# Optimization experiments

Measured on AMD Instinct MI355X. Metric: run time of the kernel, lower is better.

## Reference

```python
import jax, jax.numpy as jnp
import numpy as np

# Band partition of the 2049 frequency bins (BSRNN-style: narrow low bands, wide high bands)
_WIDTHS = [25] * 10 + [50] * 12 + [100] * 8 + [399]
_STARTS = np.concatenate([[0], np.cumsum(_WIDTHS)])
SUBBANDS = [(int(_STARTS[i]), int(_STARTS[i + 1])) for i in range(len(_WIDTHS))]
C_IN = 2          # stereo complex input channels
OUT_CH = 128      # band embedding dim
EPS = 1e-5        # GroupNorm eps
TOTAL_CH = sum(2 * C_IN * (e - s) for s, e in SUBBANDS)  # 8196


def setup_inputs() -> dict:
    key = jax.random.key(0)
    k1, k2, k3, k4 = jax.random.split(key, 4)
    B, F, T = 8, 2049, 512
    # x is view_as_real of a complex spectrogram: [B, C, F, T, 2]
    x = jax.random.normal(k1, (B, C_IN, F, T), dtype=jnp.float32)
    x = jnp.stack([x, jax.random.normal(k2, (B, C_IN, F, T), dtype=jnp.float32)], axis=-1)
    gamma = jax.random.uniform(k3, (TOTAL_CH,), dtype=jnp.float32)            # GroupNorm weight (concat over bands)
    beta = jax.random.normal(k4, (TOTAL_CH,), dtype=jnp.float32) * 0.1       # GroupNorm bias
    W = jax.random.normal(jax.random.fold_in(key, 5), (OUT_CH, TOTAL_CH), dtype=jnp.float32) * 0.02  # 1x1 conv weights, concat over bands
    b = jax.random.normal(jax.random.fold_in(key, 6), (len(SUBBANDS), OUT_CH), dtype=jnp.float32) * 0.02
    return {"x": x, "gamma": gamma, "beta": beta, "W": W, "b": b}


def reference(x, gamma, beta, W, b):
    # x: [B, C, F, T, 2] (real view of complex spectrogram)
    B, C, F, T, _ = x.shape
    outs = []
    off = 0
    for i, (s, e) in enumerate(SUBBANDS):
        ch = 2 * C * (e - s)
        # moveaxis(-1, 1): [B, 2, C, w, T] -> reshape [B, 2*C*w, T]
        h = jnp.moveaxis(x[:, :, s:e, :, :], -1, 1).reshape(B, ch, T)
        # GroupNorm(1, ch): normalize over (channel, time) per sample
        mu = jnp.mean(h, axis=(1, 2), keepdims=True)
        var = jnp.var(h, axis=(1, 2), keepdims=True)
        g = gamma[off:off + ch][None, :, None]
        bt = beta[off:off + ch][None, :, None]
        hn = (h - mu) * jax.lax.rsqrt(var + EPS) * g + bt
        # 1x1 Conv1d == per-timestep linear: [out, ch] x [B, ch, T] -> [B, out, T]
        y = jnp.einsum('oc,bct->bot', W[:, off:off + ch], hn) + b[i][None, :, None]
        outs.append(y)
        off += ch
    return jnp.stack(outs, axis=2)  # [B, OUT_CH, n_bands, T]
```

## Files before the change

### kernel.cpp

```cpp
#include <hip/hip_runtime.h>
#include <hip/hip_bf16.h>

typedef __attribute__((ext_vector_type(8))) short short8;
typedef __attribute__((ext_vector_type(4))) float f32x4;

#define NBANDS 31
#define BB 8
#define CCH 2
#define FF 2049
#define TTS 512
#define OUTC 128
#define TCH 8196
#define EPSV 1e-5f

__constant__ int c_wid[NBANDS] = {
    25,25,25,25,25,25,25,25,25,25,
    50,50,50,50,50,50,50,50,50,50,50,50,
    100,100,100,100,100,100,100,100,
    399};
__constant__ int c_start[NBANDS] = {
    0,25,50,75,100,125,150,175,200,225,
    250,300,350,400,450,500,550,600,650,700,750,800,
    850,950,1050,1150,1250,1350,1450,1550,
    1650};
__constant__ int c_cumf[NBANDS + 1] = {
    0,1,2,3,4,5,6,7,8,9,
    10,12,14,16,18,20,22,24,26,28,30,32,
    34,38,42,46,50,54,58,62,
    66,79};
__constant__ int c_kpad[NBANDS] = {
    128,128,128,128,128,128,128,128,128,128,
    256,256,256,256,256,256,256,256,256,256,256,256,
    448,448,448,448,448,448,448,448,
    1600};
__constant__ int c_kbase[NBANDS] = {
    0,16384,32768,49152,65536,81920,98304,114688,131072,147456,
    163840,196608,229376,262144,294912,327680,360448,393216,425984,458752,491520,524288,
    557056,614400,671744,729088,786432,843776,901120,958464,
    1015808};
__constant__ int c_order[NBANDS] = {
    30,22,23,24,25,26,27,28,29,
    10,11,12,13,14,15,16,17,18,19,20,21,
    0,1,2,3,4,5,6,7,8,9};

#define NSTATS 1264
#define NWPREP 248
#define NWP2   992

__device__ inline unsigned short f2bf(float f) {
    __hip_bfloat16 h = __float2bfloat16(f);
    unsigned short u;
    __builtin_memcpy(&u, &h, 2);
    return u;
}

__device__ inline void gload_lds16(const void* g, void* l) {
    __builtin_amdgcn_global_load_lds((const __attribute__((address_space(1))) void*)g,
                                     (__attribute__((address_space(3))) void*)l, 16, 0, 0);
}

__global__ __launch_bounds__(256) void prep(const float* __restrict__ x,
                                            const float* __restrict__ W,
                                            const float* __restrict__ gamma,
                                            const float* __restrict__ beta,
                                            const float* __restrict__ bias,
                                            float* __restrict__ st,
                                            float* __restrict__ wgam,
                                            float* __restrict__ wcb,
                                            unsigned short* __restrict__ wgP) {
    __shared__ float s1[256], s2[256];
    const int bid = blockIdx.x;
    const int tid = threadIdx.x;

    if (bid < NSTATS) {
        int bx  = bid >> 4;
        int ycc = bid & 15;
        int band = 0;
        while (band + 1 < NBANDS && bx >= c_cumf[band + 1]) band++;
        int fc = bx - c_cumf[band];
        int b  = ycc >> 1;
        int cc = ycc & 1;
        int w = c_wid[band], s = c_start[band];
        int f0 = fc * 32;
        int rows = min(32, w - f0);

        const float4* p = (const float4*)(x + ((size_t)(b * CCH + cc) * FF + (s + f0)) * (TTS * 2));
        int n4 = rows * 256;
        float sum = 0.f, sq = 0.f;
        for (int i = tid; i < n4; i += 256) {
            float4 v = p[i];
            sum += v.x + v.y + v.z + v.w;
            sq  += v.x * v.x + v.y * v.y + v.z * v.z + v.w * v.w;
        }
        s1[tid] = sum; s2[tid] = sq;
        __syncthreads();
        for (int st_ = 128; st_ > 0; st_ >>= 1) {
            if (tid < st_) { s1[tid] += s1[tid + st_]; s2[tid] += s2[tid + st_]; }
            __syncthreads();
        }
        if (tid == 0) {
            float* dst = st + (size_t)(bx * 16 + ycc) * 2;
            dst[0] = s1[0];
            dst[1] = s2[0];
        }
    } else if (bid < NSTATS + NWPREP) {
        int r = bid - NSTATS;
        int band = r >> 3;
        int off = 4 * c_start[band];
        int ch  = 4 * c_wid[band];
        int o = (r & 7) * 16 + (tid >> 4);
        int lane = tid & 15;
        const float* wrow = W + (size_t)o * TCH + off;
        float sg = 0.f, sb = 0.f;
        for (int c = lane; c < ch; c += 16) {
            float wv = wrow[c];
            sg += wv * gamma[off + c];
            sb += wv * beta[off + c];
        }
        for (int m = 8; m; m >>= 1) {
            sg += __shfl_down(sg, m, 16);
            sb += __shfl_down(sb, m, 16);
        }
        if (lane == 0) {
            wgam[band * OUTC + o] = sg;
            wcb[band * OUTC + o]  = sb + bias[band * OUTC + o];
        }
    } else {
        int r = bid - (NSTATS + NWPREP);
        int band = r % NBANDS;
        int gy   = r / NBANDS;
        int w = c_wid[band];
        int s4 = 4 * c_start[band];
        int Kpad = c_kpad[band];
        int base = c_kbase[band];
        int K4 = 4 * w;
        int N = OUTC * Kpad;
        for (int idx = gy * 256 + tid; idx < N; idx += 32 * 256) {
            int o = idx / Kpad;
            int k = idx - o * Kpad;
            float val = 0.f;
            if (k < K4) {
                int ri = k & 1, p = k >> 1;
                int cc = (p >= w) ? 1 : 0;
                int f = p - cc * w;
                int c = s4 + ri * 2 * w + cc * w + f;
                val = W[(size_t)o * TCH + c] * gamma[c];
            }
            int slot = (k >> 3) & 7;
            int pos = (k >> 6) * 8192 + o * 64 + ((slot ^ (o & 7)) * 8) + (k & 7);
            wgP[base + pos] = f2bf(val);
        }
    }
}

__global__ __launch_bounds__(256) void gemm_mfma(const float* __restrict__ x,
                                                 const unsigned short* __restrict__ wgP,
                                                 const float* __restrict__ st,
                                                 const float* __restrict__ wgam,
                                                 const float* __restrict__ wcb,
                                                 float* __restrict__ out) {
    const int band = c_order[blockIdx.y];
    const int b    = blockIdx.x >> 2;
    const int tt0  = (blockIdx.x & 3) * 128;
    const int w    = c_wid[band];
    const int s    = c_start[band];
    const int w2   = 2 * w;
    const int Kpad = c_kpad[band];
    const int nch  = Kpad >> 6;
    const unsigned short* wgA = wgP + c_kbase[band];

    __shared__ unsigned short lA[2][8192];

    const int tid  = threadIdx.x;
    const int lane = tid & 63;
    const int wv   = tid >> 6;
    const int l15  = lane & 15;
    const int lg   = lane >> 4;

    const float* xb = x + (size_t)b * (CCH * FF * TTS * 2);
    const float* colbase = xb + (size_t)(tt0 + wv * 32 + l15) * 2;

    f32x4 acc[8][2] = {};
    float2 bA[16], bB[16];

#define LOADB(c, dst) do {                                                     \
    _Pragma("unroll")                                                          \
    for (int kk = 0; kk < 2; ++kk)                                             \
        _Pragma("unroll")                                                      \
        for (int nf = 0; nf < 2; ++nf)                                         \
            _Pragma("unroll")                                                  \
            for (int j = 0; j < 4; ++j) {                                      \
                int p = 32 * (c) + 16 * kk + 4 * lg + j;                       \
                p = min(p, w2 - 1);                                            \
                int row = s + p + ((p >= w) ? (FF - w) : 0);                   \
                dst[kk * 8 + nf * 4 + j] =                                     \
                    *(const float2*)(colbase + (size_t)row * 1024 + nf * 32);  \
            }                                                                  \
} while (0)

#define STAGE(c, buf) do {                                                     \
    const unsigned short* srcc = wgA + (size_t)(c) * 8192;                     \
    _Pragma("unroll")                                                          \
    for (int q = 0; q < 4; ++q)                                                \
        gload_lds16(srcc + q * 2048 + tid * 8, &lA[buf][q * 2048 + tid * 8]);  \
} while (0)

#define COMPUTE(br, buf) do {                                                  \
    _Pragma("unroll")                                                          \
    for (int kk = 0; kk < 2; ++kk) {                                           \
        short8 af[8];                                                          \
        _Pragma("unroll")                                                      \
        for (int m = 0; m < 8; ++m) {                                          \
            int o = m * 16 + l15;                                              \
            int slot = (lg + 4 * kk) ^ (o & 7);                                \
            af[m] = *(const short8*)&lA[buf][o * 64 + slot * 8];               \
        }                                                                      \
        _Pragma("unroll")                                                      \
        for (int nf = 0; nf < 2; ++nf) {                                       \
            short8 bf;                                                         \
            _Pragma("unroll")                                                  \
            for (int j = 0; j < 4; ++j) {                                      \
                float2 v = br[kk * 8 + nf * 4 + j];                            \
                bf[2 * j]     = (short)f2bf(v.x);                              \
                bf[2 * j + 1] = (short)f2bf(v.y);                              \
            }                                                                  \
            _Pragma("unroll")                                                  \
            for (int m = 0; m < 8; ++m)                                        \
                acc[m][nf] = __builtin_amdgcn_mfma_f32_16x16x32_bf16(          \
                    af[m], bf, acc[m][nf], 0, 0, 0);                           \
        }                                                                      \
    }                                                                          \
} while (0)

    LOADB(0, bA);
    STAGE(0, 0);
    __syncthreads();
    for (int c = 0; c < nch; c += 2) {
        if (c + 1 < nch) { LOADB(c + 1, bB); STAGE(c + 1, 1); }
        COMPUTE(bA, 0);
        __syncthreads();
        if (c + 1 < nch) {
            if (c + 2 < nch) { LOADB(c + 2, bA); STAGE(c + 2, 0); }
            COMPUTE(bB, 1);
            __syncthreads();
        }
    }
#undef LOADB
#undef STAGE
#undef COMPUTE

    float sum = 0.f, sq = 0.f;
    {
        int c0 = c_cumf[band], c1 = c_cumf[band + 1];
        for (int c = c0; c < c1; ++c) {
            const float* p0 = st + (size_t)(c * 16 + b * 2) * 2;
            sum += p0[0] + p0[2];
            sq  += p0[1] + p0[3];
        }
    }
    const float Nf = (float)(w * 2048);
    const float mu = sum / Nf;
    const float rs = rsqrtf(sq / Nf - mu * mu + EPSV);

#pragma unroll
    for (int m = 0; m < 8; ++m) {
#pragma unroll
        for (int r = 0; r < 4; ++r) {
            int o = m * 16 + lg * 4 + r;
            float wg = wgam[band * OUTC + o];
            float cb = wcb[band * OUTC + o];
            size_t rowoff = (((size_t)b * OUTC + o) * NBANDS + band) * TTS;
#pragma unroll
            for (int nf = 0; nf < 2; ++nf) {
                int t = tt0 + wv * 32 + nf * 16 + l15;
                out[rowoff + t] = rs * (acc[m][nf][r] - mu * wg) + cb;
            }
        }
    }
}

extern "C" void kernel_launch(void* const* d_in, const int* in_sizes, int n_in,
                              void* d_out, int out_size, void* d_ws, size_t ws_size,
                              hipStream_t stream) {
    const float* x     = (const float*)d_in[0];
    const float* gamma = (const float*)d_in[1];
    const float* beta  = (const float*)d_in[2];
    const float* W     = (const float*)d_in[3];
    const float* bias  = (const float*)d_in[4];
    float* out = (float*)d_out;
    float* ws  = (float*)d_ws;

    float* st_part = ws;
    float* wgam    = ws + 3072;
    float* wcb     = ws + 7168;
    unsigned short* wgP = (unsigned short*)(ws + 11264);

    prep<<<NSTATS + NWPREP + NWP2, 256, 0, stream>>>(x, W, gamma, beta, bias,
                                                     st_part, wgam, wcb, wgP);
    gemm_mfma<<<dim3(32, NBANDS), 256, 0, stream>>>(x, wgP, st_part, wgam, wcb, out);
}
```

Baseline: 92.72 us.

## Cut register pressure in MFMA GEMM to raise occupancy, drop B double-buffer

Adds a min-blocks-per-SM hint of 4 to the GEMM launch bounds and removes the second register buffer for B operands. The B register prefetch now happens after compute instead of overlapping with it, while the LDS stage for A stays double-buffered. The inner MFMA loop loads one A fragment at a time and reuses both converted B fragments, which shortens live ranges. The aim is more resident waves to hide latency; the cost is that global loads of x are no longer overlapped with MFMA work inside a wave.

```diff
diff --git a/kernel.cpp b/kernel.cpp
--- a/kernel.cpp
+++ b/kernel.cpp
@@ -153,7 +153,7 @@
     }
 }
 
-__global__ __launch_bounds__(256) void gemm_mfma(const float* __restrict__ x,
+__global__ __launch_bounds__(256, 4) void gemm_mfma(const float* __restrict__ x,
                                                  const unsigned short* __restrict__ wgP,
                                                  const float* __restrict__ st,
                                                  const float* __restrict__ wgam,
@@ -181,7 +181,7 @@
     const float* colbase = xb + (size_t)(tt0 + wv * 32 + l15) * 2;
 
     f32x4 acc[8][2] = {};
-    float2 bA[16], bB[16];
+    float2 bA[16];
 
 #define LOADB(c, dst) do {                                                     \
     _Pragma("unroll")                                                          \
@@ -208,26 +208,25 @@
 #define COMPUTE(br, buf) do {                                                  \
     _Pragma("unroll")                                                          \
     for (int kk = 0; kk < 2; ++kk) {                                           \
-        short8 af[8];                                                          \
+        short8 bf0, bf1;                                                       \
+        _Pragma("unroll")                                                      \
+        for (int j = 0; j < 4; ++j) {                                          \
+            float2 v0 = br[kk * 8 + j];                                        \
+            float2 v1 = br[kk * 8 + 4 + j];                                    \
+            bf0[2 * j]     = (short)f2bf(v0.x);                                \
+            bf0[2 * j + 1] = (short)f2bf(v0.y);                                \
+            bf1[2 * j]     = (short)f2bf(v1.x);                                \
+            bf1[2 * j + 1] = (short)f2bf(v1.y);                                \
+        }                                                                      \
         _Pragma("unroll")                                                      \
         for (int m = 0; m < 8; ++m) {                                          \
             int o = m * 16 + l15;                                              \
             int slot = (lg + 4 * kk) ^ (o & 7);                                \
-            af[m] = *(const short8*)&lA[buf][o * 64 + slot * 8];               \
-        }                                                                      \
-        _Pragma("unroll")                                                      \
-        for (int nf = 0; nf < 2; ++nf) {                                       \
-            short8 bf;                                                         \
-            _Pragma("unroll")                                                  \
-            for (int j = 0; j < 4; ++j) {                                      \
-                float2 v = br[kk * 8 + nf * 4 + j];                            \
-                bf[2 * j]     = (short)f2bf(v.x);                              \
-                bf[2 * j + 1] = (short)f2bf(v.y);                              \
-            }                                                                  \
-            _Pragma("unroll")                                                  \
-            for (int m = 0; m < 8; ++m)                                        \
-                acc[m][nf] = __builtin_amdgcn_mfma_f32_16x16x32_bf16(          \
-                    af[m], bf, acc[m][nf], 0, 0, 0);                           \
+            short8 af = *(const short8*)&lA[buf][o * 64 + slot * 8];           \
+            acc[m][0] = __builtin_amdgcn_mfma_f32_16x16x32_bf16(               \
+                af, bf0, acc[m][0], 0, 0, 0);                                  \
+            acc[m][1] = __builtin_amdgcn_mfma_f32_16x16x32_bf16(               \
+                af, bf1, acc[m][1], 0, 0, 0);                                  \
         }                                                                      \
     }                                                                          \
 } while (0)
@@ -235,13 +234,11 @@
     LOADB(0, bA);
     STAGE(0, 0);
     __syncthreads();
-    for (int c = 0; c < nch; c += 2) {
-        if (c + 1 < nch) { LOADB(c + 1, bB); STAGE(c + 1, 1); }
-        COMPUTE(bA, 0);
-        __syncthreads();
+    for (int c = 0; c < nch; ++c) {
+        if (c + 1 < nch) STAGE(c + 1, (c + 1) & 1);
+        COMPUTE(bA, c & 1);
         if (c + 1 < nch) {
-            if (c + 2 < nch) { LOADB(c + 2, bA); STAGE(c + 2, 0); }
-            COMPUTE(bB, 1);
+            LOADB(c + 1, bA);
             __syncthreads();
         }
     }
```

Measured after the change: 97.87 us. 1.06x slower.

## Split-K the widest band across five blocks with a separate reduction kernel

Applied to the files above, without the earlier changes.

The 399-wide band needs 25 K-chunks while other bands need at most 7, so its blocks form a long tail in the GEMM grid. That band's K loop is now split over five block rows, each writing partial accumulators to workspace. A new reduce30 kernel sums the partials and applies the normalization and bias epilogue. This adds a kernel launch and extra partial-sum global traffic in exchange for better load balance.

```diff
diff --git a/kernel.cpp b/kernel.cpp
--- a/kernel.cpp
+++ b/kernel.cpp
@@ -38,10 +38,18 @@
     163840,196608,229376,262144,294912,327680,360448,393216,425984,458752,491520,524288,
     557056,614400,671744,729088,786432,843776,901120,958464,
     1015808};
-__constant__ int c_order[NBANDS] = {
-    30,22,23,24,25,26,27,28,29,
+
+#define NGY 35
+__constant__ int g_band[NGY] = {
+    30,30,30,30,30,
+    22,23,24,25,26,27,28,29,
     10,11,12,13,14,15,16,17,18,19,20,21,
     0,1,2,3,4,5,6,7,8,9};
+__constant__ int g_c0[NGY] = {
+    0,5,10,15,20,
+    0,0,0,0,0,0,0,0,
+    0,0,0,0,0,0,0,0,0,0,0,0,
+    0,0,0,0,0,0,0,0,0,0};
 
 #define NSTATS 1264
 #define NWPREP 248
@@ -158,15 +166,17 @@
                                                  const float* __restrict__ st,
                                                  const float* __restrict__ wgam,
                                                  const float* __restrict__ wcb,
+                                                 float* __restrict__ part,
                                                  float* __restrict__ out) {
-    const int band = c_order[blockIdx.y];
+    const int band = g_band[blockIdx.y];
+    const int c0   = g_c0[blockIdx.y];
     const int b    = blockIdx.x >> 2;
-    const int tt0  = (blockIdx.x & 3) * 128;
+    const int tti  = blockIdx.x & 3;
+    const int tt0  = tti * 128;
     const int w    = c_wid[band];
     const int s    = c_start[band];
     const int w2   = 2 * w;
-    const int Kpad = c_kpad[band];
-    const int nch  = Kpad >> 6;
+    const int nch  = (band == 30) ? 5 : (c_kpad[band] >> 6);
     const unsigned short* wgA = wgP + c_kbase[band];
 
     __shared__ unsigned short lA[2][8192];
@@ -232,15 +242,16 @@
     }                                                                          \
 } while (0)
 
-    LOADB(0, bA);
-    STAGE(0, 0);
+    LOADB(c0, bA);
+    STAGE(c0, 0);
     __syncthreads();
-    for (int c = 0; c < nch; c += 2) {
-        if (c + 1 < nch) { LOADB(c + 1, bB); STAGE(c + 1, 1); }
+    for (int ci = 0; ci < nch; ci += 2) {
+        int c = c0 + ci;
+        if (ci + 1 < nch) { LOADB(c + 1, bB); STAGE(c + 1, 1); }
         COMPUTE(bA, 0);
         __syncthreads();
-        if (c + 1 < nch) {
-            if (c + 2 < nch) { LOADB(c + 2, bA); STAGE(c + 2, 0); }
+        if (ci + 1 < nch) {
+            if (ci + 2 < nch) { LOADB(c + 2, bA); STAGE(c + 2, 0); }
             COMPUTE(bB, 1);
             __syncthreads();
         }
@@ -249,10 +260,24 @@
 #undef STAGE
 #undef COMPUTE
 
+    if (band == 30) {
+        float* pp = part + (((size_t)blockIdx.y * 8 + b) * 4 + tti) * 16384;
+#pragma unroll
+        for (int m = 0; m < 8; ++m)
+#pragma unroll
+            for (int r = 0; r < 4; ++r) {
+                int o = m * 16 + lg * 4 + r;
+#pragma unroll
+                for (int nf = 0; nf < 2; ++nf)
+                    pp[o * 128 + wv * 32 + nf * 16 + l15] = acc[m][nf][r];
+            }
+        return;
+    }
+
     float sum = 0.f, sq = 0.f;
     {
-        int c0 = c_cumf[band], c1 = c_cumf[band + 1];
-        for (int c = c0; c < c1; ++c) {
+        int cc0 = c_cumf[band], cc1 = c_cumf[band + 1];
+        for (int c = cc0; c < cc1; ++c) {
             const float* p0 = st + (size_t)(c * 16 + b * 2) * 2;
             sum += p0[0] + p0[2];
             sq  += p0[1] + p0[3];
@@ -276,6 +301,46 @@
                 out[rowoff + t] = rs * (acc[m][nf][r] - mu * wg) + cb;
             }
         }
+    }
+}
+
+__global__ __launch_bounds__(256) void reduce30(const float* __restrict__ st,
+                                                const float* __restrict__ wgam,
+                                                const float* __restrict__ wcb,
+                                                const float* __restrict__ part,
+                                                float* __restrict__ out) {
+    const int b   = blockIdx.x >> 2;
+    const int tti = blockIdx.x & 3;
+    const int tid = threadIdx.x;
+
+    float sum = 0.f, sq = 0.f;
+    for (int c = 66; c < 79; ++c) {
+        const float* p0 = st + (size_t)(c * 16 + b * 2) * 2;
+        sum += p0[0] + p0[2];
+        sq  += p0[1] + p0[3];
+    }
+    const float Nf = 399.f * 2048.f;
+    const float mu = sum / Nf;
+    const float rs = rsqrtf(sq / Nf - mu * mu + EPSV);
+
+    const f32x4* p4 = (const f32x4*)part;
+    const size_t sl = ((size_t)b * 4 + tti) * 4096;
+#pragma unroll
+    for (int i = 0; i < 16; ++i) {
+        int v = i * 256 + tid;
+        int o = v >> 5;
+        int tv = v & 31;
+        f32x4 a = p4[sl + v];
+        a += p4[1 * 32 * 4096 + sl + v];
+        a += p4[2 * 32 * 4096 + sl + v];
+        a += p4[3 * 32 * 4096 + sl + v];
+        a += p4[4 * 32 * 4096 + sl + v];
+        float wg = wgam[30 * OUTC + o];
+        float cb = wcb[30 * OUTC + o];
+        f32x4 y;
+#pragma unroll
+        for (int q = 0; q < 4; ++q) y[q] = rs * (a[q] - mu * wg) + cb;
+        *(f32x4*)&out[(((size_t)b * OUTC + o) * NBANDS + 30) * TTS + tti * 128 + tv * 4] = y;
     }
 }
 
@@ -294,8 +359,10 @@
     float* wgam    = ws + 3072;
     float* wcb     = ws + 7168;
     unsigned short* wgP = (unsigned short*)(ws + 11264);
+    float* part    = ws + 622592;
 
     prep<<<NSTATS + NWPREP + NWP2, 256, 0, stream>>>(x, W, gamma, beta, bias,
                                                      st_part, wgam, wcb, wgP);
-    gemm_mfma<<<dim3(32, NBANDS), 256, 0, stream>>>(x, wgP, st_part, wgam, wcb, out);
-}
+    gemm_mfma<<<dim3(32, NGY), 256, 0, stream>>>(x, wgP, st_part, wgam, wcb, part, out);
+    reduce30<<<32, 256, 0, stream>>>(st_part, wgam, wcb, part, out);
+}
```

Result: slower. 104.4 us (+12.6%).

## Convert x to bf16 MFMA-fragment tiles in stats pass, read them in GEMM

Applied to the files above, without the earlier changes.

The stats pass now also converts the input spectrogram to bf16 and writes it into a tiled layout matching the MFMA B-fragment order. The weight packing is reindexed to the new 16-frequency-block K ordering. The GEMM then loads one short8 per fragment instead of gathering strided float2 values and converting them per iteration. This halves the bytes the GEMM reads and removes conversion work from its inner loop, at the cost of an extra write and read of a bf16 copy of x through the workspace.

```diff
diff --git a/kernel.cpp b/kernel.cpp
--- a/kernel.cpp
+++ b/kernel.cpp
@@ -12,6 +12,7 @@
 #define OUTC 128
 #define TCH 8196
 #define EPSV 1e-5f
+#define NTILES 298
 
 __constant__ int c_wid[NBANDS] = {
     25,25,25,25,25,25,25,25,25,25,
@@ -38,6 +39,11 @@
     163840,196608,229376,262144,294912,327680,360448,393216,425984,458752,491520,524288,
     557056,614400,671744,729088,786432,843776,901120,958464,
     1015808};
+__constant__ int tb16b[NBANDS] = {
+    0,4,8,12,16,20,24,28,32,36,
+    40,48,56,64,72,80,88,96,104,112,120,128,
+    136,150,164,178,192,206,220,234,
+    248};
 __constant__ int c_order[NBANDS] = {
     30,22,23,24,25,26,27,28,29,
     10,11,12,13,14,15,16,17,18,19,20,21,
@@ -67,7 +73,8 @@
                                             float* __restrict__ st,
                                             float* __restrict__ wgam,
                                             float* __restrict__ wcb,
-                                            unsigned short* __restrict__ wgP) {
+                                            unsigned short* __restrict__ wgP,
+                                            unsigned short* __restrict__ xb16) {
     __shared__ float s1[256], s2[256];
     const int bid = blockIdx.x;
     const int tid = threadIdx.x;
@@ -81,16 +88,35 @@
         int b  = ycc >> 1;
         int cc = ycc & 1;
         int w = c_wid[band], s = c_start[band];
-        int f0 = fc * 32;
-        int rows = min(32, w - f0);
-
-        const float4* p = (const float4*)(x + ((size_t)(b * CCH + cc) * FF + (s + f0)) * (TTS * 2));
-        int n4 = rows * 256;
+        int nfb = (w + 15) >> 4;
+        int fb0 = fc * 2;
+        int nfbl = min(2, nfb - fb0);
+
+        int lane = tid & 63, l15 = lane & 15, lg = lane >> 4;
+        int tquad = tid >> 6;
+        const float* xcc = x + (size_t)(b * CCH + cc) * FF * 1024;
+
         float sum = 0.f, sq = 0.f;
-        for (int i = tid; i < n4; i += 256) {
-            float4 v = p[i];
-            sum += v.x + v.y + v.z + v.w;
-            sq  += v.x * v.x + v.y * v.y + v.z * v.z + v.w * v.w;
+        int ntg = nfbl * 8;
+        for (int tg = 0; tg < ntg; ++tg) {
+            int tile = tg * 4 + tquad;
+            int tb = tile & 31, fbl = tile >> 5;
+            int fb = fb0 + fbl;
+            int t = tb * 16 + l15;
+            short8 v8;
+#pragma unroll
+            for (int rr = 0; rr < 4; ++rr) {
+                int f = fb * 16 + 4 * lg + rr;
+                float2 v = make_float2(0.f, 0.f);
+                if (f < w)
+                    v = *(const float2*)(xcc + (size_t)(s + f) * 1024 + t * 2);
+                sum += v.x + v.y;
+                sq  += v.x * v.x + v.y * v.y;
+                v8[2 * rr]     = (short)f2bf(v.x);
+                v8[2 * rr + 1] = (short)f2bf(v.y);
+            }
+            int taug = tb16b[band] + fb * 2 + cc;
+            *(short8*)(xb16 + (((size_t)b * NTILES + taug) * 32 + tb) * 512 + lane * 8) = v8;
         }
         s1[tid] = sum; s2[tid] = sq;
         __syncthreads();
@@ -133,16 +159,15 @@
         int s4 = 4 * c_start[band];
         int Kpad = c_kpad[band];
         int base = c_kbase[band];
-        int K4 = 4 * w;
         int N = OUTC * Kpad;
         for (int idx = gy * 256 + tid; idx < N; idx += 32 * 256) {
             int o = idx / Kpad;
             int k = idx - o * Kpad;
+            int tau = k >> 5, fb = tau >> 1, cc = tau & 1;
+            int fo = (k & 31) >> 1, ri = k & 1;
+            int f = fb * 16 + fo;
             float val = 0.f;
-            if (k < K4) {
-                int ri = k & 1, p = k >> 1;
-                int cc = (p >= w) ? 1 : 0;
-                int f = p - cc * w;
+            if (f < w) {
                 int c = s4 + ri * 2 * w + cc * w + f;
                 val = W[(size_t)o * TCH + c] * gamma[c];
             }
@@ -153,7 +178,7 @@
     }
 }
 
-__global__ __launch_bounds__(256) void gemm_mfma(const float* __restrict__ x,
+__global__ __launch_bounds__(256) void gemm_mfma(const unsigned short* __restrict__ xb16,
                                                  const unsigned short* __restrict__ wgP,
                                                  const float* __restrict__ st,
                                                  const float* __restrict__ wgam,
@@ -161,12 +186,10 @@
                                                  float* __restrict__ out) {
     const int band = c_order[blockIdx.y];
     const int b    = blockIdx.x >> 2;
-    const int tt0  = (blockIdx.x & 3) * 128;
+    const int tti  = blockIdx.x & 3;
+    const int tt0  = tti * 128;
     const int w    = c_wid[band];
-    const int s    = c_start[band];
-    const int w2   = 2 * w;
-    const int Kpad = c_kpad[band];
-    const int nch  = Kpad >> 6;
+    const int nch  = c_kpad[band] >> 6;
     const unsigned short* wgA = wgP + c_kbase[band];
 
     __shared__ unsigned short lA[2][8192];
@@ -177,25 +200,19 @@
     const int l15  = lane & 15;
     const int lg   = lane >> 4;
 
-    const float* xb = x + (size_t)b * (CCH * FF * TTS * 2);
-    const float* colbase = xb + (size_t)(tt0 + wv * 32 + l15) * 2;
+    const unsigned short* xbT = xb16 +
+        (((size_t)b * NTILES + tb16b[band]) * 32 + tti * 8 + wv * 2) * 512 + lane * 8;
 
     f32x4 acc[8][2] = {};
-    float2 bA[16], bB[16];
+    short8 bA[4], bB[4];
 
 #define LOADB(c, dst) do {                                                     \
     _Pragma("unroll")                                                          \
     for (int kk = 0; kk < 2; ++kk)                                             \
         _Pragma("unroll")                                                      \
         for (int nf = 0; nf < 2; ++nf)                                         \
-            _Pragma("unroll")                                                  \
-            for (int j = 0; j < 4; ++j) {                                      \
-                int p = 32 * (c) + 16 * kk + 4 * lg + j;                       \
-                p = min(p, w2 - 1);                                            \
-                int row = s + p + ((p >= w) ? (FF - w) : 0);                   \
-                dst[kk * 8 + nf * 4 + j] =                                     \
-                    *(const float2*)(colbase + (size_t)row * 1024 + nf * 32);  \
-            }                                                                  \
+            dst[kk * 2 + nf] =                                                 \
+                *(const short8*)(xbT + (size_t)((2 * (c) + kk) * 32 + nf) * 512); \
 } while (0)
 
 #define STAGE(c, buf) do {                                                     \
@@ -216,19 +233,11 @@
             af[m] = *(const short8*)&lA[buf][o * 64 + slot * 8];               \
         }                                                                      \
         _Pragma("unroll")                                                      \
-        for (int nf = 0; nf < 2; ++nf) {                                       \
-            short8 bf;                                                         \
-            _Pragma("unroll")                                                  \
-            for (int j = 0; j < 4; ++j) {                                      \
-                float2 v = br[kk * 8 + nf * 4 + j];                            \
-                bf[2 * j]     = (short)f2bf(v.x);                              \
-                bf[2 * j + 1] = (short)f2bf(v.y);                              \
-            }                                                                  \
+        for (int nf = 0; nf < 2; ++nf)                                         \
             _Pragma("unroll")                                                  \
             for (int m = 0; m < 8; ++m)                                        \
                 acc[m][nf] = __builtin_amdgcn_mfma_f32_16x16x32_bf16(          \
-                    af[m], bf, acc[m][nf], 0, 0, 0);                           \
-        }                                                                      \
+                    af[m], br[kk * 2 + nf], acc[m][nf], 0, 0, 0);              \
     }                                                                          \
 } while (0)
 
@@ -251,8 +260,8 @@
 
     float sum = 0.f, sq = 0.f;
     {
-        int c0 = c_cumf[band], c1 = c_cumf[band + 1];
-        for (int c = c0; c < c1; ++c) {
+        int cc0 = c_cumf[band], cc1 = c_cumf[band + 1];
+        for (int c = cc0; c < cc1; ++c) {
             const float* p0 = st + (size_t)(c * 16 + b * 2) * 2;
             sum += p0[0] + p0[2];
             sq  += p0[1] + p0[3];
@@ -293,9 +302,10 @@
     float* st_part = ws;
     float* wgam    = ws + 3072;
     float* wcb     = ws + 7168;
-    unsigned short* wgP = (unsigned short*)(ws + 11264);
+    unsigned short* wgP  = (unsigned short*)(ws + 11264);
+    unsigned short* xb16 = (unsigned short*)(ws + 622592);
 
     prep<<<NSTATS + NWPREP + NWP2, 256, 0, stream>>>(x, W, gamma, beta, bias,
-                                                     st_part, wgam, wcb, wgP);
-    gemm_mfma<<<dim3(32, NBANDS), 256, 0, stream>>>(x, wgP, st_part, wgam, wcb, out);
-}
+                                                     st_part, wgam, wcb, wgP, xb16);
+    gemm_mfma<<<dim3(32, NBANDS), 256, 0, stream>>>(xb16, wgP, st_part, wgam, wcb, out);
+}
```

Result: slower. 98.09 us (+5.8%).
